# Optimization experiments

Hardware: AMD Instinct MI355X
Metric: run time of the kernel (lower is better)

Reference implementation:

```python
import jax, jax.numpy as jnp
import numpy as np

N_NODES = 50000
N_EDGES = 1000000
C = 32          # nchannels (multiplicity of each irrep)
NBESSEL = 8
WEIGHT_NUMEL = 3 * C  # three uvu paths: 0e->0e, 0e->1o, 0e->2e


def setup_inputs() -> dict:
    key = jax.random.key(0)
    ks = jax.random.split(key, 12)
    inp = {
        "lenght": jax.random.uniform(ks[0], (N_EDGES, NBESSEL), dtype=jnp.float32),
        "node_features": jax.random.normal(ks[1], (N_NODES, C), dtype=jnp.float32),
        "edge_attributes": jax.random.normal(ks[2], (N_EDGES, 9), dtype=jnp.float32),
        "edge_index": jax.random.randint(ks[3], (2, N_EDGES), 0, N_NODES, dtype=jnp.int64),
        # FullyConnectedNet([8, 6, 6, 6, 96]) weights (e3nn stores unnormalized W, divides by sqrt(fan_in))
        "fcn_w0": jax.random.normal(ks[4], (NBESSEL, 6), dtype=jnp.float32),
        "fcn_w1": jax.random.normal(ks[5], (6, 6), dtype=jnp.float32),
        "fcn_w2": jax.random.normal(ks[6], (6, 6), dtype=jnp.float32),
        "fcn_w3": jax.random.normal(ks[7], (6, WEIGHT_NUMEL), dtype=jnp.float32),
        # equivariant Linear irreps_mid -> irreps_out: one [C, C] mixing matrix per l in {0,1,2}
        "lin_w0": jax.random.normal(ks[8], (C, C), dtype=jnp.float32),
        "lin_w1": jax.random.normal(ks[9], (C, C), dtype=jnp.float32),
        "lin_w2": jax.random.normal(ks[10], (C, C), dtype=jnp.float32),
    }
    return inp


def _fcn(x, w0, w1, w2, w3):
    # e3nn FullyConnectedNet: normalized linear layers with SiLU on hidden layers
    for w in (w0, w1, w2):
        x = jax.nn.silu((x @ w) * (1.0 / np.float32(np.sqrt(w.shape[0]))))
    return (x @ w3) * (1.0 / np.float32(np.sqrt(w3.shape[0])))


def reference(lenght, node_features, edge_attributes, edge_index,
              fcn_w0, fcn_w1, fcn_w2, fcn_w3, lin_w0, lin_w1, lin_w2):
    sender = edge_index[0]
    receiver = edge_index[1]
    num_nodes = node_features.shape[0]
    c = node_features.shape[1]
    e = lenght.shape[0]

    # per-edge tensor-product weights: [E, 3C]
    tp_w = _fcn(lenght, fcn_w0, fcn_w1, fcn_w2, fcn_w3)
    w0, w1, w2 = tp_w[:, :c], tp_w[:, c:2 * c], tp_w[:, 2 * c:]

    x = node_features[sender]                       # gather: [E, C]
    y0 = edge_attributes[:, 0:1]                    # 0e: [E, 1]
    y1 = edge_attributes[:, 1:4]                    # 1o: [E, 3]
    y2 = edge_attributes[:, 4:9]                    # 2e: [E, 5]

    # uvu tensor product, CG for 0e x l -> l is identity
    m0 = w0 * x * y0                                # [E, C]
    m1 = (w1 * x)[:, :, None] * y1[:, None, :]      # [E, C, 3]
    m2 = (w2 * x)[:, :, None] * y2[:, None, :]      # [E, C, 5]
    mij = jnp.concatenate(
        [m0, m1.reshape(e, 3 * c), m2.reshape(e, 5 * c)], axis=1)  # [E, 9C]

    # scatter_sum over receivers
    msg = jax.ops.segment_sum(mij, receiver, num_segments=num_nodes)  # [N, 9C]

    # equivariant Linear (per-l channel mixing, 1/sqrt(fan_in) normalization)
    inv = 1.0 / np.float32(np.sqrt(c))
    o0 = (msg[:, :c] @ lin_w0) * inv                                   # [N, C]
    o1 = jnp.einsum('nci,cd->ndi', msg[:, c:4 * c].reshape(num_nodes, c, 3), lin_w1) * inv
    o2 = jnp.einsum('nci,cd->ndi', msg[:, 4 * c:].reshape(num_nodes, c, 5), lin_w2) * inv
    return jnp.concatenate(
        [o0, o1.reshape(num_nodes, 3 * c), o2.reshape(num_nodes, 5 * c)], axis=1)
```

## Files before the change

kernel.cpp:

```cpp
#include <hip/hip_runtime.h>
#include <math.h>

#define N_NODES 50000
#define N_EDGES 1000000
#define CCH     32
#define ROW     288
#define SCAN_BLOCKS 196
#define REC_PAD 64

__global__ __launch_bounds__(256) void rank_kernel(
    const int* __restrict__ edge_index, int* __restrict__ deg,
    int* __restrict__ rank)
{
    const int e = blockIdx.x * 256 + threadIdx.x;
    if (e >= N_EDGES) return;
    rank[e] = atomicAdd(&deg[edge_index[N_EDGES + e]], 1);
}

__global__ __launch_bounds__(256) void scan_local_kernel(
    const int* __restrict__ deg, int* __restrict__ lexcl, int* __restrict__ blocksum)
{
    __shared__ int s[256];
    const int t = threadIdx.x;
    const int gid = blockIdx.x * 256 + t;
    const int v = (gid < N_NODES) ? deg[gid] : 0;
    s[t] = v;
    __syncthreads();
    for (int ofs = 1; ofs < 256; ofs <<= 1) {
        int w = (t >= ofs) ? s[t - ofs] : 0;
        __syncthreads();
        s[t] += w;
        __syncthreads();
    }
    if (gid < N_NODES) lexcl[gid] = s[t] - v;
    if (t == 255) blocksum[blockIdx.x] = s[255];
}

__global__ __launch_bounds__(256) void scan_top_kernel(
    const int* __restrict__ blocksum, int* __restrict__ blockpref)
{
    __shared__ int s[256];
    const int t = threadIdx.x;
    const int v = (t < SCAN_BLOCKS) ? blocksum[t] : 0;
    s[t] = v;
    __syncthreads();
    for (int ofs = 1; ofs < 256; ofs <<= 1) {
        int w = (t >= ofs) ? s[t - ofs] : 0;
        __syncthreads();
        s[t] += w;
        __syncthreads();
    }
    if (t < SCAN_BLOCKS) blockpref[t] = s[t] - v;
}

__global__ __launch_bounds__(256) void scan_addback_kernel(
    const int* __restrict__ lexcl, const int* __restrict__ blockpref,
    int* __restrict__ offset)
{
    const int gid = blockIdx.x * 256 + threadIdx.x;
    if (gid >= N_NODES) return;
    offset[gid] = blockpref[blockIdx.x] + lexcl[gid];
}

__global__ __launch_bounds__(256) void pack_kernel(
    const float* __restrict__ lenght,
    const float* __restrict__ edge_attr,
    const int*   __restrict__ edge_index,
    const float* __restrict__ fw0,
    const float* __restrict__ fw1,
    const float* __restrict__ fw2,
    const int*   __restrict__ offset,
    const int*   __restrict__ rank,
    float4*      __restrict__ rec)
{
    __shared__ float s_w[120];
    __shared__ float s_ea[256 * 9];
    for (int i = threadIdx.x; i < 120; i += 256)
        s_w[i] = (i < 48) ? fw0[i] : (i < 84) ? fw1[i - 48] : fw2[i - 84];
    {
        const int base_dw = blockIdx.x * (256 * 9);
        #pragma unroll
        for (int k = 0; k < 9; ++k) {
            const int i = k * 256 + threadIdx.x;
            const int g = base_dw + i;
            if (g < 9 * N_EDGES) s_ea[i] = edge_attr[g];
        }
    }
    __syncthreads();
    const float* sw0 = s_w;
    const float* sw1 = s_w + 48;
    const float* sw2 = s_w + 84;

    const int e = blockIdx.x * 256 + threadIdx.x;
    if (e >= N_EDGES) return;

    const float inv8 = 0.35355339059327373f;
    const float inv6 = 0.4082482904638631f;

    float len[8];
    const float4 l0 = ((const float4*)(lenght + (long long)e * 8))[0];
    const float4 l1 = ((const float4*)(lenght + (long long)e * 8))[1];
    len[0]=l0.x; len[1]=l0.y; len[2]=l0.z; len[3]=l0.w;
    len[4]=l1.x; len[5]=l1.y; len[6]=l1.z; len[7]=l1.w;

    float h0[6], h1[6], h2[6];
    #pragma unroll
    for (int j = 0; j < 6; ++j) {
        float a = 0.f;
        #pragma unroll
        for (int k = 0; k < 8; ++k) a += len[k] * sw0[k * 6 + j];
        a *= inv8;
        h0[j] = a / (1.f + __expf(-a));
    }
    #pragma unroll
    for (int j = 0; j < 6; ++j) {
        float a = 0.f;
        #pragma unroll
        for (int k = 0; k < 6; ++k) a += h0[k] * sw1[k * 6 + j];
        a *= inv6;
        h1[j] = a / (1.f + __expf(-a));
    }
    #pragma unroll
    for (int j = 0; j < 6; ++j) {
        float a = 0.f;
        #pragma unroll
        for (int k = 0; k < 6; ++k) a += h1[k] * sw2[k * 6 + j];
        a *= inv6;
        h2[j] = a * inv6 / (1.f + __expf(-a));
    }

    const float* ea = s_ea + threadIdx.x * 9;
    float y[9];
    #pragma unroll
    for (int i = 0; i < 9; ++i) y[i] = ea[i];

    const int snd = edge_index[e];
    const int r   = edge_index[N_EDGES + e];
    const int p   = offset[r] + rank[e];

    float4* rp = rec + (long long)p * 4;
    rp[0] = make_float4(h2[0], h2[1], h2[2], h2[3]);
    rp[1] = make_float4(h2[4], h2[5], y[0], y[1]);
    rp[2] = make_float4(y[2], y[3], y[4], y[5]);
    rp[3] = make_float4(y[6], y[7], y[8], __int_as_float(snd));
}

#define EDGE_ACC(Ra,Rb,Rc,Rd,xx) do {                                          \
    const float w0c_ = Ra.x*f3a[0] + Ra.y*f3a[1] + Ra.z*f3a[2]                 \
                     + Ra.w*f3a[3] + Rb.x*f3a[4] + Rb.y*f3a[5];                \
    const float w1c_ = Ra.x*f3b[0] + Ra.y*f3b[1] + Ra.z*f3b[2]                 \
                     + Ra.w*f3b[3] + Rb.x*f3b[4] + Rb.y*f3b[5];                \
    const float w2c_ = Ra.x*f3c[0] + Ra.y*f3c[1] + Ra.z*f3c[2]                 \
                     + Ra.w*f3c[3] + Rb.x*f3c[4] + Rb.y*f3c[5];                \
    acc[0] += (w0c_ * (xx)) * Rb.z;                                            \
    const float a1_ = w1c_ * (xx);                                             \
    acc[1] += a1_ * Rb.w; acc[2] += a1_ * Rc.x; acc[3] += a1_ * Rc.y;          \
    const float a2_ = w2c_ * (xx);                                             \
    acc[4] += a2_ * Rc.z; acc[5] += a2_ * Rc.w;                                \
    acc[6] += a2_ * Rd.x; acc[7] += a2_ * Rd.y; acc[8] += a2_ * Rd.z;          \
} while (0)

__global__ __launch_bounds__(128) void gather_kernel(
    const float4* __restrict__ rec,
    const float*  __restrict__ node_features,
    const int*    __restrict__ offset,
    const int*    __restrict__ deg,
    const float*  __restrict__ fw3,
    const float*  __restrict__ lw0,
    const float*  __restrict__ lw1,
    const float*  __restrict__ lw2,
    float*        __restrict__ out)
{
    __shared__ float s_m[2][384];

    const int wave = threadIdx.x >> 6;
    const int l    = threadIdx.x & 63;
    const int c    = l & 31;
    const int h    = l >> 5;
    const int node = blockIdx.x * 2 + wave;

    float f3a[6], f3b[6], f3c[6];
    #pragma unroll
    for (int k = 0; k < 6; ++k) {
        f3a[k] = fw3[k * 96 + c];
        f3b[k] = fw3[k * 96 + 32 + c];
        f3c[k] = fw3[k * 96 + 64 + c];
    }

    int off = offset[node];
    int dg  = deg[node];
    off = __builtin_amdgcn_readfirstlane(off);
    dg  = __builtin_amdgcn_readfirstlane(dg);
    const int nph = (dg + 3) >> 2;

    const float4* rb = rec + (size_t)off * 4;

    float acc[9] = {0.f,0.f,0.f,0.f,0.f,0.f,0.f,0.f,0.f};

    if (nph > 0) {
        int jA = 2 * h;
        int jB = 2 * h + 4;

        float4 A0 = rb[4*jA+0], A1 = rb[4*jA+1], A2 = rb[4*jA+2], A3 = rb[4*jA+3];
        float4 A4 = rb[4*jA+4], A5 = rb[4*jA+5], A6 = rb[4*jA+6], A7 = rb[4*jA+7];
        float4 B0 = rb[4*jB+0], B1 = rb[4*jB+1], B2 = rb[4*jB+2], B3 = rb[4*jB+3];
        float4 B4 = rb[4*jB+4], B5 = rb[4*jB+5], B6 = rb[4*jB+6], B7 = rb[4*jB+7];
        float xAr0 = node_features[(size_t)__float_as_int(A3.w) * CCH + c];
        float xAr1 = node_features[(size_t)__float_as_int(A7.w) * CCH + c];
        bool  vA0 = (jA < dg), vA1 = (jA + 1 < dg);
        float xBr0 = 0.f, xBr1 = 0.f;
        bool  vB0 = false, vB1 = false;

        int p = 0;
        while (true) {
            {
                const float xA0 = vA0 ? xAr0 : 0.f;
                const float xA1 = vA1 ? xAr1 : 0.f;
                EDGE_ACC(A0, A1, A2, A3, xA0);
                EDGE_ACC(A4, A5, A6, A7, xA1);
                xBr0 = node_features[(size_t)__float_as_int(B3.w) * CCH + c];
                xBr1 = node_features[(size_t)__float_as_int(B7.w) * CCH + c];
                vB0 = (jB < dg); vB1 = (jB + 1 < dg);
                jA += 8;
                A0 = rb[4*jA+0]; A1 = rb[4*jA+1]; A2 = rb[4*jA+2]; A3 = rb[4*jA+3];
                A4 = rb[4*jA+4]; A5 = rb[4*jA+5]; A6 = rb[4*jA+6]; A7 = rb[4*jA+7];
                if (++p == nph) break;
            }
            {
                const float xB0 = vB0 ? xBr0 : 0.f;
                const float xB1 = vB1 ? xBr1 : 0.f;
                EDGE_ACC(B0, B1, B2, B3, xB0);
                EDGE_ACC(B4, B5, B6, B7, xB1);
                xAr0 = node_features[(size_t)__float_as_int(A3.w) * CCH + c];
                xAr1 = node_features[(size_t)__float_as_int(A7.w) * CCH + c];
                vA0 = (jA < dg); vA1 = (jA + 1 < dg);
                jB += 8;
                B0 = rb[4*jB+0]; B1 = rb[4*jB+1]; B2 = rb[4*jB+2]; B3 = rb[4*jB+3];
                B4 = rb[4*jB+4]; B5 = rb[4*jB+5]; B6 = rb[4*jB+6]; B7 = rb[4*jB+7];
                if (++p == nph) break;
            }
        }
    }

    #pragma unroll
    for (int k = 0; k < 9; ++k) acc[k] += __shfl_down(acc[k], 32);

    if (h == 0) {
        float4* mp = (float4*)&s_m[wave][c * 12];
        mp[0] = make_float4(acc[0], acc[1], acc[2], acc[3]);
        mp[1] = make_float4(acc[4], acc[5], acc[6], acc[7]);
        s_m[wave][c * 12 + 8] = acc[8];
    }
    asm volatile("s_waitcnt lgkmcnt(0)" ::: "memory");

    const int d = c;
    float o0 = 0.f;
    float o1[3] = {0.f, 0.f, 0.f};
    float o2[5] = {0.f, 0.f, 0.f, 0.f, 0.f};
    for (int cc = h * 16; cc < h * 16 + 16; ++cc) {
        const float4 ma = *(const float4*)&s_m[wave][cc * 12];
        const float4 mb = *(const float4*)&s_m[wave][cc * 12 + 4];
        const float  m8 = s_m[wave][cc * 12 + 8];
        o0 += ma.x * lw0[cc * 32 + d];
        const float w1 = lw1[cc * 32 + d];
        o1[0] += ma.y * w1; o1[1] += ma.z * w1; o1[2] += ma.w * w1;
        const float w2 = lw2[cc * 32 + d];
        o2[0] += mb.x * w2; o2[1] += mb.y * w2; o2[2] += mb.z * w2;
        o2[3] += mb.w * w2; o2[4] += m8   * w2;
    }

    o0 += __shfl_down(o0, 32);
    #pragma unroll
    for (int i = 0; i < 3; ++i) o1[i] += __shfl_down(o1[i], 32);
    #pragma unroll
    for (int i = 0; i < 5; ++i) o2[i] += __shfl_down(o2[i], 32);

    if (h == 0) {
        const float inv32 = 0.17677669529663687f;
        float* rw = &s_m[wave][0];
        rw[d] = o0 * inv32;
        #pragma unroll
        for (int i = 0; i < 3; ++i) rw[32 + d * 3 + i] = o1[i] * inv32;
        #pragma unroll
        for (int i = 0; i < 5; ++i) rw[128 + d * 5 + i] = o2[i] * inv32;
    }
    asm volatile("s_waitcnt lgkmcnt(0)" ::: "memory");

    const float4* rowp = (const float4*)&s_m[wave][0];
    float4* op4 = (float4*)(out + (size_t)node * ROW);
    op4[l] = rowp[l];
    if (l < 8) op4[64 + l] = rowp[64 + l];
}

extern "C" void kernel_launch(void* const* d_in, const int* in_sizes, int n_in,
                              void* d_out, int out_size, void* d_ws, size_t ws_size,
                              hipStream_t stream)
{
    const float* lenght = (const float*)d_in[0];
    const float* nf     = (const float*)d_in[1];
    const float* ea     = (const float*)d_in[2];
    const int*   ei     = (const int*)d_in[3];
    const float* fw0    = (const float*)d_in[4];
    const float* fw1    = (const float*)d_in[5];
    const float* fw2    = (const float*)d_in[6];
    const float* fw3    = (const float*)d_in[7];
    const float* lw0    = (const float*)d_in[8];
    const float* lw1    = (const float*)d_in[9];
    const float* lw2    = (const float*)d_in[10];
    float* out = (float*)d_out;

    char* ws = (char*)d_ws;
    float4* rec    = (float4*)ws; ws += ((size_t)N_EDGES * 4 + REC_PAD) * sizeof(float4);
    int* rank      = (int*)ws;    ws += (size_t)N_EDGES * sizeof(int);
    int* deg       = (int*)ws;    ws += (size_t)N_NODES * sizeof(int);
    int* offset    = (int*)ws;    ws += (size_t)N_NODES * sizeof(int);
    int* lexcl     = (int*)ws;    ws += (size_t)N_NODES * sizeof(int);
    int* blocksum  = (int*)ws;    ws += (size_t)SCAN_BLOCKS * sizeof(int);
    int* blockpref = (int*)ws;    ws += (size_t)SCAN_BLOCKS * sizeof(int);
    float4* recpad = rec + (size_t)N_EDGES * 4;

    hipMemsetAsync(deg, 0, (size_t)N_NODES * sizeof(int), stream);
    hipMemsetAsync(recpad, 0, (size_t)REC_PAD * sizeof(float4), stream);

    const int EB = (N_EDGES + 255) / 256;
    rank_kernel        <<<EB, 256, 0, stream>>>(ei, deg, rank);
    scan_local_kernel  <<<SCAN_BLOCKS, 256, 0, stream>>>(deg, lexcl, blocksum);
    scan_top_kernel    <<<1, 256, 0, stream>>>(blocksum, blockpref);
    scan_addback_kernel<<<SCAN_BLOCKS, 256, 0, stream>>>(lexcl, blockpref, offset);
    pack_kernel        <<<EB, 256, 0, stream>>>(lenght, ea, ei, fw0, fw1, fw2,
                                                offset, rank, rec);
    gather_kernel      <<<N_NODES / 2, 128, 0, stream>>>(
        rec, nf, offset, deg, fw3, lw0, lw1, lw2, out);
}
```

Before: 337.0 us.

## Fuse CSR build stages into one cooperative kernel with grid syncs

Replaces the two memsets plus five build kernels (rank, three scan stages, pack) with a single cooperative kernel of 1024 blocks that separates the phases with grid-wide syncs and uses grid-stride loops. The aim is to cut the launch overhead and inter-kernel gaps of many small dependent launches. In exchange, each phase now runs on a fixed grid that may be smaller than the edge count needs, grid.sync itself has a cost, and the old multi-kernel path is kept as a fallback if the cooperative launch fails.

```diff
diff --git a/kernel.cpp b/kernel.cpp
--- a/kernel.cpp
+++ b/kernel.cpp
@@ -1,5 +1,8 @@
 #include <hip/hip_runtime.h>
+#include <hip/hip_cooperative_groups.h>
 #include <math.h>
+
+namespace cg = cooperative_groups;
 
 #define N_NODES 50000
 #define N_EDGES 1000000
@@ -7,6 +10,154 @@
 #define ROW     288
 #define SCAN_BLOCKS 196
 #define REC_PAD 64
+#define BUILD_BLOCKS 1024
+
+__device__ __forceinline__ void mlp_pack_one(
+    const float* __restrict__ lenght, const float* __restrict__ ea9,
+    const int* __restrict__ edge_index,
+    const float* sw0, const float* sw1, const float* sw2,
+    int e, int p, float4* __restrict__ rec)
+{
+    const float inv8 = 0.35355339059327373f;
+    const float inv6 = 0.4082482904638631f;
+
+    float len[8];
+    const float4 l0 = ((const float4*)(lenght + (long long)e * 8))[0];
+    const float4 l1 = ((const float4*)(lenght + (long long)e * 8))[1];
+    len[0]=l0.x; len[1]=l0.y; len[2]=l0.z; len[3]=l0.w;
+    len[4]=l1.x; len[5]=l1.y; len[6]=l1.z; len[7]=l1.w;
+
+    float h0[6], h1[6], h2[6];
+    #pragma unroll
+    for (int j = 0; j < 6; ++j) {
+        float a = 0.f;
+        #pragma unroll
+        for (int k = 0; k < 8; ++k) a += len[k] * sw0[k * 6 + j];
+        a *= inv8;
+        h0[j] = a / (1.f + __expf(-a));
+    }
+    #pragma unroll
+    for (int j = 0; j < 6; ++j) {
+        float a = 0.f;
+        #pragma unroll
+        for (int k = 0; k < 6; ++k) a += h0[k] * sw1[k * 6 + j];
+        a *= inv6;
+        h1[j] = a / (1.f + __expf(-a));
+    }
+    #pragma unroll
+    for (int j = 0; j < 6; ++j) {
+        float a = 0.f;
+        #pragma unroll
+        for (int k = 0; k < 6; ++k) a += h1[k] * sw2[k * 6 + j];
+        a *= inv6;
+        h2[j] = a * inv6 / (1.f + __expf(-a));
+    }
+
+    float y[9];
+    #pragma unroll
+    for (int i = 0; i < 9; ++i) y[i] = ea9[i];
+
+    const int snd = edge_index[e];
+
+    float4* rp = rec + (long long)p * 4;
+    rp[0] = make_float4(h2[0], h2[1], h2[2], h2[3]);
+    rp[1] = make_float4(h2[4], h2[5], y[0], y[1]);
+    rp[2] = make_float4(y[2], y[3], y[4], y[5]);
+    rp[3] = make_float4(y[6], y[7], y[8], __int_as_float(snd));
+}
+
+__global__ __launch_bounds__(256) void build_kernel(
+    const float* __restrict__ lenght,
+    const float* __restrict__ edge_attr,
+    const int*   __restrict__ edge_index,
+    const float* __restrict__ fw0,
+    const float* __restrict__ fw1,
+    const float* __restrict__ fw2,
+    int*         __restrict__ deg,
+    int*         __restrict__ rank,
+    int*         __restrict__ offset,
+    int*         __restrict__ lexcl,
+    int*         __restrict__ blocksum,
+    int*         __restrict__ blockpref,
+    float4*      __restrict__ rec)
+{
+    cg::grid_group grid = cg::this_grid();
+
+    __shared__ int   s_i[256];
+    __shared__ float s_w[120];
+    __shared__ float s_ea[256 * 9];
+
+    const int t   = threadIdx.x;
+    const int tid = blockIdx.x * 256 + t;
+    const int NT  = gridDim.x * 256;
+
+    for (int i = tid; i < N_NODES; i += NT) deg[i] = 0;
+    {
+        float4* recpad = rec + (size_t)N_EDGES * 4;
+        if (tid < REC_PAD) recpad[tid] = make_float4(0.f, 0.f, 0.f, 0.f);
+    }
+    grid.sync();
+
+    for (int e = tid; e < N_EDGES; e += NT)
+        rank[e] = atomicAdd(&deg[edge_index[N_EDGES + e]], 1);
+    grid.sync();
+
+    if (blockIdx.x < SCAN_BLOCKS) {
+        const int gid = blockIdx.x * 256 + t;
+        const int v = (gid < N_NODES) ? deg[gid] : 0;
+        s_i[t] = v;
+        __syncthreads();
+        for (int ofs = 1; ofs < 256; ofs <<= 1) {
+            int w = (t >= ofs) ? s_i[t - ofs] : 0;
+            __syncthreads();
+            s_i[t] += w;
+            __syncthreads();
+        }
+        if (gid < N_NODES) lexcl[gid] = s_i[t] - v;
+        if (t == 255) blocksum[blockIdx.x] = s_i[255];
+    }
+    grid.sync();
+
+    if (blockIdx.x == 0) {
+        const int v = (t < SCAN_BLOCKS) ? blocksum[t] : 0;
+        s_i[t] = v;
+        __syncthreads();
+        for (int ofs = 1; ofs < 256; ofs <<= 1) {
+            int w = (t >= ofs) ? s_i[t - ofs] : 0;
+            __syncthreads();
+            s_i[t] += w;
+            __syncthreads();
+        }
+        if (t < SCAN_BLOCKS) blockpref[t] = s_i[t] - v;
+    }
+    grid.sync();
+
+    for (int i = tid; i < N_NODES; i += NT)
+        offset[i] = blockpref[i >> 8] + lexcl[i];
+    grid.sync();
+
+    for (int i = t; i < 120; i += 256)
+        s_w[i] = (i < 48) ? fw0[i] : (i < 84) ? fw1[i - 48] : fw2[i - 84];
+    const int NTILES = (N_EDGES + 255) / 256;
+    for (int tile = blockIdx.x; tile < NTILES; tile += gridDim.x) {
+        __syncthreads();
+        const int base_dw = tile * (256 * 9);
+        #pragma unroll
+        for (int k = 0; k < 9; ++k) {
+            const int i = k * 256 + t;
+            const int g = base_dw + i;
+            if (g < 9 * N_EDGES) s_ea[i] = edge_attr[g];
+        }
+        __syncthreads();
+        const int e = tile * 256 + t;
+        if (e < N_EDGES) {
+            const int r = edge_index[N_EDGES + e];
+            const int p = offset[r] + rank[e];
+            mlp_pack_one(lenght, s_ea + t * 9, edge_index,
+                         s_w, s_w + 48, s_w + 84, e, p, rec);
+        }
+    }
+}
 
 __global__ __launch_bounds__(256) void rank_kernel(
     const int* __restrict__ edge_index, int* __restrict__ deg,
@@ -63,15 +214,12 @@
 }
 
 __global__ __launch_bounds__(256) void pack_kernel(
-    const float* __restrict__ lenght,
-    const float* __restrict__ edge_attr,
-    const int*   __restrict__ edge_index,
-    const float* __restrict__ fw0,
-    const float* __restrict__ fw1,
+    const float* __restrict__ lenght, const float* __restrict__ edge_attr,
+    const int* __restrict__ edge_index,
+    const float* __restrict__ fw0, const float* __restrict__ fw1,
     const float* __restrict__ fw2,
-    const int*   __restrict__ offset,
-    const int*   __restrict__ rank,
-    float4*      __restrict__ rec)
+    const int* __restrict__ offset, const int* __restrict__ rank,
+    float4* __restrict__ rec)
 {
     __shared__ float s_w[120];
     __shared__ float s_ea[256 * 9];
@@ -87,62 +235,13 @@
         }
     }
     __syncthreads();
-    const float* sw0 = s_w;
-    const float* sw1 = s_w + 48;
-    const float* sw2 = s_w + 84;
 
     const int e = blockIdx.x * 256 + threadIdx.x;
     if (e >= N_EDGES) return;
-
-    const float inv8 = 0.35355339059327373f;
-    const float inv6 = 0.4082482904638631f;
-
-    float len[8];
-    const float4 l0 = ((const float4*)(lenght + (long long)e * 8))[0];
-    const float4 l1 = ((const float4*)(lenght + (long long)e * 8))[1];
-    len[0]=l0.x; len[1]=l0.y; len[2]=l0.z; len[3]=l0.w;
-    len[4]=l1.x; len[5]=l1.y; len[6]=l1.z; len[7]=l1.w;
-
-    float h0[6], h1[6], h2[6];
-    #pragma unroll
-    for (int j = 0; j < 6; ++j) {
-        float a = 0.f;
-        #pragma unroll
-        for (int k = 0; k < 8; ++k) a += len[k] * sw0[k * 6 + j];
-        a *= inv8;
-        h0[j] = a / (1.f + __expf(-a));
-    }
-    #pragma unroll
-    for (int j = 0; j < 6; ++j) {
-        float a = 0.f;
-        #pragma unroll
-        for (int k = 0; k < 6; ++k) a += h0[k] * sw1[k * 6 + j];
-        a *= inv6;
-        h1[j] = a / (1.f + __expf(-a));
-    }
-    #pragma unroll
-    for (int j = 0; j < 6; ++j) {
-        float a = 0.f;
-        #pragma unroll
-        for (int k = 0; k < 6; ++k) a += h1[k] * sw2[k * 6 + j];
-        a *= inv6;
-        h2[j] = a * inv6 / (1.f + __expf(-a));
-    }
-
-    const float* ea = s_ea + threadIdx.x * 9;
-    float y[9];
-    #pragma unroll
-    for (int i = 0; i < 9; ++i) y[i] = ea[i];
-
-    const int snd = edge_index[e];
-    const int r   = edge_index[N_EDGES + e];
-    const int p   = offset[r] + rank[e];
-
-    float4* rp = rec + (long long)p * 4;
-    rp[0] = make_float4(h2[0], h2[1], h2[2], h2[3]);
-    rp[1] = make_float4(h2[4], h2[5], y[0], y[1]);
-    rp[2] = make_float4(y[2], y[3], y[4], y[5]);
-    rp[3] = make_float4(y[6], y[7], y[8], __int_as_float(snd));
+    const int r = edge_index[N_EDGES + e];
+    const int p = offset[r] + rank[e];
+    mlp_pack_one(lenght, s_ea + threadIdx.x * 9, edge_index,
+                 s_w, s_w + 48, s_w + 84, e, p, rec);
 }
 
 #define EDGE_ACC(Ra,Rb,Rc,Rd,xx) do {                                          \
@@ -319,16 +418,27 @@
     int* blockpref = (int*)ws;    ws += (size_t)SCAN_BLOCKS * sizeof(int);
     float4* recpad = rec + (size_t)N_EDGES * 4;
 
-    hipMemsetAsync(deg, 0, (size_t)N_NODES * sizeof(int), stream);
-    hipMemsetAsync(recpad, 0, (size_t)REC_PAD * sizeof(float4), stream);
-
-    const int EB = (N_EDGES + 255) / 256;
-    rank_kernel        <<<EB, 256, 0, stream>>>(ei, deg, rank);
-    scan_local_kernel  <<<SCAN_BLOCKS, 256, 0, stream>>>(deg, lexcl, blocksum);
-    scan_top_kernel    <<<1, 256, 0, stream>>>(blocksum, blockpref);
-    scan_addback_kernel<<<SCAN_BLOCKS, 256, 0, stream>>>(lexcl, blockpref, offset);
-    pack_kernel        <<<EB, 256, 0, stream>>>(lenght, ea, ei, fw0, fw1, fw2,
-                                                offset, rank, rec);
-    gather_kernel      <<<N_NODES / 2, 128, 0, stream>>>(
+    void* kargs[] = {
+        (void*)&lenght, (void*)&ea, (void*)&ei,
+        (void*)&fw0, (void*)&fw1, (void*)&fw2,
+        (void*)&deg, (void*)&rank, (void*)&offset,
+        (void*)&lexcl, (void*)&blocksum, (void*)&blockpref, (void*)&rec
+    };
+    hipError_t rc = hipLaunchCooperativeKernel(
+        (void*)build_kernel, dim3(BUILD_BLOCKS), dim3(256), kargs, 0, stream);
+
+    if (rc != hipSuccess) {
+        hipMemsetAsync(deg, 0, (size_t)N_NODES * sizeof(int), stream);
+        hipMemsetAsync(recpad, 0, (size_t)REC_PAD * sizeof(float4), stream);
+        const int EB = (N_EDGES + 255) / 256;
+        rank_kernel        <<<EB, 256, 0, stream>>>(ei, deg, rank);
+        scan_local_kernel  <<<SCAN_BLOCKS, 256, 0, stream>>>(deg, lexcl, blocksum);
+        scan_top_kernel    <<<1, 256, 0, stream>>>(blocksum, blockpref);
+        scan_addback_kernel<<<SCAN_BLOCKS, 256, 0, stream>>>(lexcl, blockpref, offset);
+        pack_kernel        <<<EB, 256, 0, stream>>>(lenght, ea, ei, fw0, fw1, fw2,
+                                                    offset, rank, rec);
+    }
+
+    gather_kernel<<<N_NODES / 2, 128, 0, stream>>>(
         rec, nf, offset, deg, fw3, lw0, lw1, lw2, out);
 }
```

Result: slower. 824.0 us (+144.5%).
